# Performance work log

Hardware: AMD Instinct MI355X
Metric: run time of the kernel (lower is better)

Reference implementation:

```python
import jax, jax.numpy as jnp
import numpy as np

CODEBOOK_SIZE = 8192
EMBED_DIM = 256


def setup_inputs() -> dict:
    key = jax.random.key(0)
    k_rep, k_cb = jax.random.split(key)
    rep = jax.random.normal(k_rep, (32, 2048, EMBED_DIM), dtype=jnp.float32)
    codebook = jax.random.normal(k_cb, (CODEBOOK_SIZE, EMBED_DIM), dtype=jnp.float32)
    return {"rep": rep, "codebook": codebook}


def reference(rep, codebook):
    # rep: [B, M, D], codebook: [K, D]
    B, M, D = rep.shape
    rep_flat = rep.reshape(-1, D)                                # [B*M, D]
    a2 = jnp.sum(rep_flat * rep_flat, axis=1, keepdims=True)     # [B*M, 1]
    b2 = jnp.sum(codebook * codebook, axis=1)[None, :]           # [1, K]
    ab = rep_flat @ codebook.T                                   # [B*M, K]
    dist = a2 + b2 - 2.0 * ab                                    # [B*M, K]
    idx = jnp.argmin(dist, axis=1).reshape(B, M)                 # [B, M] int
    return idx
```

## Files before the change

kernel.cpp:

```cpp
#include <hip/hip_runtime.h>
#include <stdint.h>

#define KCODES 8192
#define DIM 256
#define BN 128
#define NKT (KCODES / BN)
#define NSTEP (NKT * 4)

typedef _Float16 h16;
typedef __attribute__((ext_vector_type(8))) _Float16 f16x8;
typedef __attribute__((ext_vector_type(4))) float f32x4;

__device__ __forceinline__ void split8(const float* __restrict__ x, f16x8& h, f16x8& l) {
    #pragma unroll
    for (int i = 0; i < 8; ++i) {
        float v = x[i];
        _Float16 hv = (_Float16)v;
        h[i] = hv;
        l[i] = (_Float16)(v - (float)hv);
    }
}

__device__ __forceinline__ unsigned int ford(float f) {
    unsigned int b = __float_as_uint(f);
    return (b & 0x80000000u) ? ~b : (b | 0x80000000u);
}

#define WS_C2H   0u
#define WS_LC    32768u
#define WS_CN    65536u
#define WS_CNT   98304u
#define WS_LIST  98560u
#define WS_CAND  360704u
#define WS_THR   622848u
#define WS_KEYS  917504u
#define WS_BPH   2097152u

__global__ __launch_bounds__(256) void c2x_kernel(const float* __restrict__ cb,
                                                  float* __restrict__ c2h,
                                                  float* __restrict__ lc,
                                                  float* __restrict__ cn, int K) {
    int w = (blockIdx.x * blockDim.x + threadIdx.x) >> 6;
    int lane = threadIdx.x & 63;
    if (w >= K) return;
    const float4 v = *(const float4*)(cb + (size_t)w * DIM + lane * 4);
    float s = 0.f, sr = 0.f;
    const float xs[4] = {v.x, v.y, v.z, v.w};
    #pragma unroll
    for (int i = 0; i < 4; ++i) {
        float x = xs[i];
        s += x * x;
        float hf = (float)(_Float16)x;
        float rho = x - hf;
        sr += rho * rho;
    }
    #pragma unroll
    for (int off = 32; off > 0; off >>= 1) { s += __shfl_down(s, off); sr += __shfl_down(sr, off); }
    if (lane == 0) { c2h[w] = 0.5f * s; cn[w] = sqrtf(s); lc[w] = sqrtf(sr); }
}

__global__ __launch_bounds__(256) void pack_h_kernel(const float* __restrict__ cb,
                                                     h16* __restrict__ Bp) {
    const int tid = blockIdx.x * 256 + threadIdx.x;
    const int code = tid >> 5;
    const int grp = tid & 31;
    float x[8];
    *(float4*)&x[0] = *(const float4*)(cb + (size_t)code * DIM + grp * 8);
    *(float4*)&x[4] = *(const float4*)(cb + (size_t)code * DIM + grp * 8 + 4);
    f16x8 hh;
    #pragma unroll
    for (int i = 0; i < 8; ++i) hh[i] = (_Float16)x[i];
    const int kt = code >> 7, col = code & 127;
    const int chunk = grp >> 2, g = grp & 3;
    const int P = kt * 4 + (chunk >> 1);
    const int s = (chunk & 1) * 4 + g;
    const int phys = s ^ (col & 7);
    *(f16x8*)(Bp + (size_t)P * 8192 + col * 64 + phys * 8) = hh;
}

__global__ __launch_bounds__(256, 3) void vq_pass1(
    const float* __restrict__ rep, const h16* __restrict__ Bp,
    const float* __restrict__ c2h, const float* __restrict__ lcA,
    const float* __restrict__ cnA, int* __restrict__ cand,
    float* __restrict__ thr) {

    __shared__ __align__(16) h16 ring[3][8192];

    const int t = threadIdx.x;
    const int lane = t & 63;
    const int c15 = lane & 15;
    const int g = lane >> 4;
    const int w = t >> 6;
    const int wrow = (w >> 1) * 32;
    const int wcol = (w & 1) * 64;
    const int row0 = blockIdx.x * 64;

    f16x8 ah[2][8];
    float hn[2], rn[2];
    #pragma unroll
    for (int m = 0; m < 2; ++m) {
        const float* ar = rep + (size_t)(row0 + wrow + m * 16 + c15) * DIM + g * 8;
        float hs = 0.f, rs = 0.f;
        #pragma unroll
        for (int ch = 0; ch < 8; ++ch) {
            float x[8];
            *(float4*)&x[0] = *(const float4*)(ar + ch * 32);
            *(float4*)&x[4] = *(const float4*)(ar + ch * 32 + 4);
            #pragma unroll
            for (int i = 0; i < 8; ++i) {
                _Float16 hv = (_Float16)x[i];
                ah[m][ch][i] = hv;
                float hf = (float)hv;
                hs += hf * hf;
                float rho = x[i] - hf;
                rs += rho * rho;
            }
        }
        hs += __shfl_xor(hs, 16); hs += __shfl_xor(hs, 32);
        rs += __shfl_xor(rs, 16); rs += __shfl_xor(rs, 32);
        hn[m] = sqrtf(hs); rn[m] = sqrtf(rs);
    }

    f32x4 acc[2][4];
    float u1v[2][4], u2v[2][4], B2[2][4];
    int u1i[2][4];
    #pragma unroll
    for (int m = 0; m < 2; ++m)
        #pragma unroll
        for (int n = 0; n < 4; ++n) {
            #pragma unroll
            for (int r = 0; r < 4; ++r) acc[m][n][r] = 0.f;
            u1v[m][n] = -3.4e38f; u2v[m][n] = -3.4e38f; u1i[m][n] = 0;
        }

    auto issueStep = [&](int s2, int slot) {
        const h16* src = Bp + (size_t)s2 * 8192 + t * 8;
        h16* dst = &ring[slot][t * 8];
        #pragma unroll
        for (int i = 0; i < 4; ++i)
            __builtin_amdgcn_global_load_lds(
                (const __attribute__((address_space(1))) uint32_t*)(src + i * 2048),
                (__attribute__((address_space(3))) uint32_t*)(dst + i * 2048),
                16, 0, 0);
    };

    asm volatile("s_waitcnt vmcnt(0)" ::: "memory");
    issueStep(0, 0);
    issueStep(1, 1);

    int bufq = 0;
    #pragma unroll 1
    for (int kt = 0; kt < NKT; ++kt) {
        const int ktbase = kt * BN;
        #pragma unroll
        for (int cp = 0; cp < 4; ++cp) {
            const int s = kt * 4 + cp;
            if (s == NSTEP - 1) asm volatile("s_waitcnt vmcnt(0) lgkmcnt(0)" ::: "memory");
            else                asm volatile("s_waitcnt vmcnt(4) lgkmcnt(0)" ::: "memory");
            __builtin_amdgcn_s_barrier();
            __builtin_amdgcn_sched_barrier(0);

            if (cp == 0) {
                #pragma unroll
                for (int n = 0; n < 4; ++n) {
                    const int col = ktbase + wcol + n * 16 + c15;
                    float cc = c2h[col], lv = lcA[col], cv = cnA[col];
                    #pragma unroll
                    for (int m = 0; m < 2; ++m)
                        B2[m][n] = hn[m] * lv + rn[m] * cv + 0.012f - cc;
                }
            }
            if (s + 2 < NSTEP) {
                int slot = bufq + 2;
                if (slot >= 3) slot -= 3;
                issueStep(s + 2, slot);
            }

            const h16* lb = &ring[bufq][0];
            #pragma unroll
            for (int j = 0; j < 2; ++j) {
                const int ch = cp * 2 + j;
                #pragma unroll
                for (int n = 0; n < 4; ++n) {
                    const int base = (wcol + n * 16 + c15) * 64;
                    f16x8 bh = *(const f16x8*)&lb[base + (((j * 4 + g) ^ (c15 & 7)) << 3)];
                    #pragma unroll
                    for (int m = 0; m < 2; ++m)
                        acc[m][n] = __builtin_amdgcn_mfma_f32_16x16x32_f16(ah[m][ch], bh, acc[m][n], 0, 0, 0);
                }
            }

            if (cp == 3) {
                #pragma unroll
                for (int n = 0; n < 4; ++n) {
                    const int col = ktbase + wcol + n * 16 + c15;
                    #pragma unroll
                    for (int m = 0; m < 2; ++m)
                        #pragma unroll
                        for (int r = 0; r < 4; ++r) {
                            float u = acc[m][n][r] + B2[m][n];
                            if (u > u1v[m][r]) { u2v[m][r] = u1v[m][r]; u1v[m][r] = u; u1i[m][r] = col; }
                            else if (u > u2v[m][r]) u2v[m][r] = u;
                            acc[m][n][r] = 0.f;
                        }
                }
            }
            bufq = (bufq + 1 == 3) ? 0 : bufq + 1;
        }
    }

    __syncthreads();
    float* sv1 = (float*)&ring[0][0];
    int* si1 = (int*)((char*)&ring[0][0] + 1024);
    float* sv2 = (float*)((char*)&ring[0][0] + 2048);
    #pragma unroll
    for (int m = 0; m < 2; ++m)
        #pragma unroll
        for (int r = 0; r < 4; ++r) {
            float a1 = u1v[m][r], a2 = u2v[m][r];
            int a1i = u1i[m][r];
            #pragma unroll
            for (int mask = 1; mask <= 8; mask <<= 1) {
                float b1 = __shfl_xor(a1, mask);
                int b1i = __shfl_xor(a1i, mask);
                float b2 = __shfl_xor(a2, mask);
                if (b1 > a1) { a2 = fmaxf(a1, b2); a1 = b1; a1i = b1i; }
                else         { a2 = fmaxf(b1, a2); }
            }
            if (c15 == 0) {
                const int rl = wrow + m * 16 + g * 4 + r;
                sv1[rl * 2 + (w & 1)] = a1;
                si1[rl * 2 + (w & 1)] = a1i;
                sv2[rl * 2 + (w & 1)] = a2;
            }
        }
    __syncthreads();
    if (t < 64) {
        float a1 = sv1[t * 2], a2 = sv2[t * 2];
        int a1i = si1[t * 2];
        float b1 = sv1[t * 2 + 1], b2 = sv2[t * 2 + 1];
        int b1i = si1[t * 2 + 1];
        float u1, u2; int u1idx;
        if (b1 > a1) { u1 = b1; u1idx = b1i; u2 = fmaxf(a1, b2); }
        else         { u1 = a1; u1idx = a1i; u2 = fmaxf(b1, a2); }
        cand[row0 + t] = u1idx;
        thr[row0 + t] = u2;
    }
}

__global__ __launch_bounds__(256) void resolve_kernel(
    const float* __restrict__ rep, const float* __restrict__ cb,
    const float* __restrict__ c2h, const int* __restrict__ cand,
    const float* __restrict__ thr, int* __restrict__ out,
    int* __restrict__ cnt, int* __restrict__ list, int N) {
    const int W = (blockIdx.x * 256 + threadIdx.x) >> 6;
    const int lane = threadIdx.x & 63;
    if (W >= N) return;
    const int ci = cand[W];
    const float4 rv = *(const float4*)(rep + (size_t)W * DIM + lane * 4);
    const float4 cv = *(const float4*)(cb + (size_t)ci * DIM + lane * 4);
    float p = rv.x * cv.x + rv.y * cv.y + rv.z * cv.z + rv.w * cv.w;
    #pragma unroll
    for (int off = 32; off > 0; off >>= 1) p += __shfl_down(p, off);
    if (lane == 0) {
        float sex = p - c2h[ci];
        out[W] = ci;
        if (!(sex > thr[W])) {
            int pos = atomicAdd(cnt, 1);
            list[pos] = W;
        }
    }
}

__global__ __launch_bounds__(256) void rescan_kernel(
    const float* __restrict__ rep, const float* __restrict__ cb,
    const float* __restrict__ c2h, const int* __restrict__ cnt_p,
    const int* __restrict__ list, unsigned long long* __restrict__ keys) {

    const int cnt = *cnt_p;
    const int base = blockIdx.x * 64;
    if (base >= cnt) return;
    const int nrows = min(64, cnt - base);
    const int ktbase = (int)blockIdx.y * BN;

    __shared__ __align__(16) h16 lds[2][BN * 64];
    const int t = threadIdx.x;
    const int lane = t & 63;
    const int w = t >> 6;
    const int c15 = lane & 15;
    const int g = lane >> 4;
    const int wrow = w * 16;

    const int aslot = wrow + c15;
    const int grow = list[base + (aslot < nrows ? aslot : 0)];
    f16x8 ah[8], al[8];
    {
        const float* ar = rep + (size_t)grow * DIM + g * 8;
        #pragma unroll
        for (int ch = 0; ch < 8; ++ch) {
            float x[8];
            *(float4*)&x[0] = *(const float4*)(ar + ch * 32);
            *(float4*)&x[4] = *(const float4*)(ar + ch * 32 + 4);
            split8(x, ah[ch], al[ch]);
        }
    }
    f32x4 acc[8];
    float cc[8];
    #pragma unroll
    for (int n = 0; n < 8; ++n) {
        #pragma unroll
        for (int r = 0; r < 4; ++r) acc[n][r] = 0.f;
        cc[n] = c2h[ktbase + n * 16 + c15];
    }

    const int scol = t >> 1;
    const int dslot = t & 1;
    float breg[16];
    auto loadB = [&](int ch) {
        const float* src = cb + (size_t)(ktbase + scol) * DIM + ch * 32 + dslot * 16;
        #pragma unroll
        for (int i = 0; i < 4; ++i) *(float4*)&breg[i * 4] = *(const float4*)(src + i * 4);
    };
    auto writeB = [&](int buf) {
        #pragma unroll
        for (int half = 0; half < 2; ++half) {
            f16x8 hh, ll;
            split8(&breg[half * 8], hh, ll);
            const int s = dslot * 2 + half;
            *(f16x8*)&lds[buf][scol * 64 + ((s ^ (scol & 7)) << 3)] = hh;
            *(f16x8*)&lds[buf][scol * 64 + (((s + 4) ^ (scol & 7)) << 3)] = ll;
        }
    };

    loadB(0);
    writeB(0);
    loadB(1);
    __syncthreads();

    #pragma unroll
    for (int chunk = 0; chunk < 8; ++chunk) {
        const int buf = chunk & 1;
        if (chunk != 7) writeB(buf ^ 1);
        if (chunk <= 5) loadB(chunk + 2);
        #pragma unroll
        for (int n = 0; n < 8; ++n) {
            const int bb = (n * 16 + c15) * 64;
            f16x8 bh = *(const f16x8*)&lds[buf][bb + ((g ^ (lane & 7)) << 3)];
            f16x8 bl = *(const f16x8*)&lds[buf][bb + (((4 + g) ^ (lane & 7)) << 3)];
            acc[n] = __builtin_amdgcn_mfma_f32_16x16x32_f16(ah[chunk], bh, acc[n], 0, 0, 0);
            acc[n] = __builtin_amdgcn_mfma_f32_16x16x32_f16(ah[chunk], bl, acc[n], 0, 0, 0);
            acc[n] = __builtin_amdgcn_mfma_f32_16x16x32_f16(al[chunk], bh, acc[n], 0, 0, 0);
            acc[n] = __builtin_amdgcn_mfma_f32_16x16x32_f16(al[chunk], bl, acc[n], 0, 0, 0);
        }
        __syncthreads();
    }

    #pragma unroll
    for (int r = 0; r < 4; ++r) {
        float bv = -3.4e38f;
        int bi = 0;
        #pragma unroll
        for (int n = 0; n < 8; ++n) {
            float s2 = acc[n][r] - cc[n];
            const int col = ktbase + n * 16 + c15;
            if (s2 > bv) { bv = s2; bi = col; }
        }
        #pragma unroll
        for (int mask = 1; mask <= 8; mask <<= 1) {
            float ov = __shfl_xor(bv, mask);
            int oi = __shfl_xor(bi, mask);
            if (ov > bv || (ov == bv && oi < bi)) { bv = ov; bi = oi; }
        }
        const int oslot = wrow + g * 4 + r;
        if (c15 == 0 && oslot < nrows) {
            unsigned long long key =
                ((unsigned long long)ford(bv) << 32) | (unsigned int)(~(unsigned int)bi);
            atomicMax(&keys[list[base + oslot]], key);
        }
    }
}

__global__ __launch_bounds__(256) void writeback_kernel(
    const int* __restrict__ cnt_p, const int* __restrict__ list,
    const unsigned long long* __restrict__ keys, int* __restrict__ out) {
    int i = blockIdx.x * 256 + threadIdx.x;
    if (i >= *cnt_p) return;
    int row = list[i];
    out[row] = (int)(~(unsigned int)(keys[row] & 0xFFFFFFFFull));
}

extern "C" void kernel_launch(void* const* d_in, const int* in_sizes, int n_in,
                              void* d_out, int out_size, void* d_ws, size_t ws_size,
                              hipStream_t stream) {
    const float* rep = (const float*)d_in[0];
    const float* cb = (const float*)d_in[1];
    const int N = in_sizes[0] / DIM;
    const int K = in_sizes[1] / DIM;
    char* ws = (char*)d_ws;
    float* c2h = (float*)(ws + WS_C2H);
    float* lc  = (float*)(ws + WS_LC);
    float* cn  = (float*)(ws + WS_CN);
    int* cnt   = (int*)(ws + WS_CNT);
    int* list  = (int*)(ws + WS_LIST);
    int* cand  = (int*)(ws + WS_CAND);
    float* thr = (float*)(ws + WS_THR);
    unsigned long long* keys = (unsigned long long*)(ws + WS_KEYS);
    h16* Bph   = (h16*)(ws + WS_BPH);
    int* out = (int*)d_out;

    c2x_kernel<<<dim3((K * 64 + 255) / 256), dim3(256), 0, stream>>>(cb, c2h, lc, cn, K);
    pack_h_kernel<<<dim3(KCODES * 32 / 256), dim3(256), 0, stream>>>(cb, Bph);
    hipMemsetAsync(cnt, 0, sizeof(int), stream);
    hipMemsetAsync(keys, 0, (size_t)N * sizeof(unsigned long long), stream);
    vq_pass1<<<dim3(N / 64), dim3(256), 0, stream>>>(rep, Bph, c2h, lc, cn, cand, thr);
    resolve_kernel<<<dim3(N / 4), dim3(256), 0, stream>>>(rep, cb, c2h, cand, thr, out, cnt, list, N);
    rescan_kernel<<<dim3(N / 64, NKT), dim3(256), 0, stream>>>(rep, cb, c2h, cnt, list, keys);
    writeback_kernel<<<dim3(N / 256), dim3(256), 0, stream>>>(cnt, list, keys, out);
}
```

Baseline: 524.8 us.

## Double rows per block and use global-max error bound in pass1

Each block in the first pass now handles 128 rows instead of 64, with each wave computing a 64x64 tile. Every LDS-loaded codebook fragment is therefore reused across four A fragments, which halves codebook traffic per row. The per-code error bound, built from per-code residual and norm values, is replaced by a row-only bound that uses the global maxima of those values, gathered with atomics in c2x. That bound is folded into the accumulator initial value, which removes per-tile bias loads and a separate add. The looser bound likely admits more ambiguous rows into the rescan path, and occupancy drops from 3 to 2 blocks because of higher register use.

```diff
diff --git a/kernel.cpp b/kernel.cpp
--- a/kernel.cpp
+++ b/kernel.cpp
@@ -39,7 +39,9 @@
 __global__ __launch_bounds__(256) void c2x_kernel(const float* __restrict__ cb,
                                                   float* __restrict__ c2h,
                                                   float* __restrict__ lc,
-                                                  float* __restrict__ cn, int K) {
+                                                  float* __restrict__ cn,
+                                                  unsigned int* __restrict__ gmx,
+                                                  int K) {
     int w = (blockIdx.x * blockDim.x + threadIdx.x) >> 6;
     int lane = threadIdx.x & 63;
     if (w >= K) return;
@@ -56,7 +58,12 @@
     }
     #pragma unroll
     for (int off = 32; off > 0; off >>= 1) { s += __shfl_down(s, off); sr += __shfl_down(sr, off); }
-    if (lane == 0) { c2h[w] = 0.5f * s; cn[w] = sqrtf(s); lc[w] = sqrtf(sr); }
+    if (lane == 0) {
+        float sn = sqrtf(s), srn = sqrtf(sr);
+        c2h[w] = 0.5f * s; cn[w] = sn; lc[w] = srn;
+        atomicMax(&gmx[0], __float_as_uint(srn));
+        atomicMax(&gmx[1], __float_as_uint(sn));
+    }
 }
 
 __global__ __launch_bounds__(256) void pack_h_kernel(const float* __restrict__ cb,
@@ -78,11 +85,10 @@
     *(f16x8*)(Bp + (size_t)P * 8192 + col * 64 + phys * 8) = hh;
 }
 
-__global__ __launch_bounds__(256, 3) void vq_pass1(
+__global__ __launch_bounds__(256, 2) void vq_pass1(
     const float* __restrict__ rep, const h16* __restrict__ Bp,
-    const float* __restrict__ c2h, const float* __restrict__ lcA,
-    const float* __restrict__ cnA, int* __restrict__ cand,
-    float* __restrict__ thr) {
+    const float* __restrict__ c2h, const unsigned int* __restrict__ gmx,
+    int* __restrict__ cand, float* __restrict__ thr) {
 
     __shared__ __align__(16) h16 ring[3][8192];
 
@@ -91,14 +97,17 @@
     const int c15 = lane & 15;
     const int g = lane >> 4;
     const int w = t >> 6;
-    const int wrow = (w >> 1) * 32;
+    const int wrow = (w >> 1) * 64;
     const int wcol = (w & 1) * 64;
-    const int row0 = blockIdx.x * 64;
-
-    f16x8 ah[2][8];
-    float hn[2], rn[2];
-    #pragma unroll
-    for (int m = 0; m < 2; ++m) {
+    const int row0 = blockIdx.x * 128;
+
+    const float Lmax = __uint_as_float(gmx[0]);
+    const float Cmax = __uint_as_float(gmx[1]);
+
+    f16x8 ah[4][8];
+    float U[4][4];
+    #pragma unroll
+    for (int m = 0; m < 4; ++m) {
         const float* ar = rep + (size_t)(row0 + wrow + m * 16 + c15) * DIM + g * 8;
         float hs = 0.f, rs = 0.f;
         #pragma unroll
@@ -118,20 +127,22 @@
         }
         hs += __shfl_xor(hs, 16); hs += __shfl_xor(hs, 32);
         rs += __shfl_xor(rs, 16); rs += __shfl_xor(rs, 32);
-        hn[m] = sqrtf(hs); rn[m] = sqrtf(rs);
-    }
-
-    f32x4 acc[2][4];
-    float u1v[2][4], u2v[2][4], B2[2][4];
-    int u1i[2][4];
-    #pragma unroll
-    for (int m = 0; m < 2; ++m)
-        #pragma unroll
-        for (int n = 0; n < 4; ++n) {
-            #pragma unroll
-            for (int r = 0; r < 4; ++r) acc[m][n][r] = 0.f;
-            u1v[m][n] = -3.4e38f; u2v[m][n] = -3.4e38f; u1i[m][n] = 0;
-        }
+        float hn = sqrtf(hs), rn = sqrtf(rs);
+        #pragma unroll
+        for (int r = 0; r < 4; ++r) {
+            float hnr = __shfl(hn, g * 4 + r);
+            float rnr = __shfl(rn, g * 4 + r);
+            U[m][r] = fmaf(hnr, Lmax, fmaf(rnr, Cmax, 0.012f));
+        }
+    }
+
+    f32x4 acc[4][4];
+    float u1v[4][4], u2v[4][4], D[4];
+    int u1i[4][4];
+    #pragma unroll
+    for (int m = 0; m < 4; ++m)
+        #pragma unroll
+        for (int r = 0; r < 4; ++r) { u1v[m][r] = -3.4e38f; u2v[m][r] = -3.4e38f; u1i[m][r] = 0; }
 
     auto issueStep = [&](int s2, int slot) {
         const h16* src = Bp + (size_t)s2 * 8192 + t * 8;
@@ -162,13 +173,13 @@
 
             if (cp == 0) {
                 #pragma unroll
-                for (int n = 0; n < 4; ++n) {
-                    const int col = ktbase + wcol + n * 16 + c15;
-                    float cc = c2h[col], lv = lcA[col], cv = cnA[col];
+                for (int n = 0; n < 4; ++n) D[n] = c2h[ktbase + wcol + n * 16 + c15];
+                #pragma unroll
+                for (int m = 0; m < 4; ++m)
                     #pragma unroll
-                    for (int m = 0; m < 2; ++m)
-                        B2[m][n] = hn[m] * lv + rn[m] * cv + 0.012f - cc;
-                }
+                    for (int n = 0; n < 4; ++n)
+                        #pragma unroll
+                        for (int r = 0; r < 4; ++r) acc[m][n][r] = U[m][r];
             }
             if (s + 2 < NSTEP) {
                 int slot = bufq + 2;
@@ -179,14 +190,15 @@
             const h16* lb = &ring[bufq][0];
             #pragma unroll
             for (int j = 0; j < 2; ++j) {
-                const int ch = cp * 2 + j;
                 #pragma unroll
                 for (int n = 0; n < 4; ++n) {
                     const int base = (wcol + n * 16 + c15) * 64;
                     f16x8 bh = *(const f16x8*)&lb[base + (((j * 4 + g) ^ (c15 & 7)) << 3)];
                     #pragma unroll
-                    for (int m = 0; m < 2; ++m)
+                    for (int m = 0; m < 4; ++m) {
+                        const int ch = cp * 2 + j;
                         acc[m][n] = __builtin_amdgcn_mfma_f32_16x16x32_f16(ah[m][ch], bh, acc[m][n], 0, 0, 0);
+                    }
                 }
             }
 
@@ -195,13 +207,12 @@
                 for (int n = 0; n < 4; ++n) {
                     const int col = ktbase + wcol + n * 16 + c15;
                     #pragma unroll
-                    for (int m = 0; m < 2; ++m)
+                    for (int m = 0; m < 4; ++m)
                         #pragma unroll
                         for (int r = 0; r < 4; ++r) {
-                            float u = acc[m][n][r] + B2[m][n];
+                            float u = acc[m][n][r] - D[n];
                             if (u > u1v[m][r]) { u2v[m][r] = u1v[m][r]; u1v[m][r] = u; u1i[m][r] = col; }
                             else if (u > u2v[m][r]) u2v[m][r] = u;
-                            acc[m][n][r] = 0.f;
                         }
                 }
             }
@@ -214,7 +225,7 @@
     int* si1 = (int*)((char*)&ring[0][0] + 1024);
     float* sv2 = (float*)((char*)&ring[0][0] + 2048);
     #pragma unroll
-    for (int m = 0; m < 2; ++m)
+    for (int m = 0; m < 4; ++m)
         #pragma unroll
         for (int r = 0; r < 4; ++r) {
             float a1 = u1v[m][r], a2 = u2v[m][r];
@@ -235,7 +246,7 @@
             }
         }
     __syncthreads();
-    if (t < 64) {
+    if (t < 128) {
         float a1 = sv1[t * 2], a2 = sv2[t * 2];
         int a1i = si1[t * 2];
         float b1 = sv1[t * 2 + 1], b2 = sv2[t * 2 + 1];
@@ -401,6 +412,7 @@
     float* lc  = (float*)(ws + WS_LC);
     float* cn  = (float*)(ws + WS_CN);
     int* cnt   = (int*)(ws + WS_CNT);
+    unsigned int* gmx = (unsigned int*)(ws + WS_CNT + 4);
     int* list  = (int*)(ws + WS_LIST);
     int* cand  = (int*)(ws + WS_CAND);
     float* thr = (float*)(ws + WS_THR);
@@ -408,11 +420,11 @@
     h16* Bph   = (h16*)(ws + WS_BPH);
     int* out = (int*)d_out;
 
-    c2x_kernel<<<dim3((K * 64 + 255) / 256), dim3(256), 0, stream>>>(cb, c2h, lc, cn, K);
+    hipMemsetAsync(ws + WS_CNT, 0, 64, stream);
+    hipMemsetAsync(keys, 0, (size_t)N * sizeof(unsigned long long), stream);
+    c2x_kernel<<<dim3((K * 64 + 255) / 256), dim3(256), 0, stream>>>(cb, c2h, lc, cn, gmx, K);
     pack_h_kernel<<<dim3(KCODES * 32 / 256), dim3(256), 0, stream>>>(cb, Bph);
-    hipMemsetAsync(cnt, 0, sizeof(int), stream);
-    hipMemsetAsync(keys, 0, (size_t)N * sizeof(unsigned long long), stream);
-    vq_pass1<<<dim3(N / 64), dim3(256), 0, stream>>>(rep, Bph, c2h, lc, cn, cand, thr);
+    vq_pass1<<<dim3(N / 128), dim3(256), 0, stream>>>(rep, Bph, c2h, gmx, cand, thr);
     resolve_kernel<<<dim3(N / 4), dim3(256), 0, stream>>>(rep, cb, c2h, cand, thr, out, cnt, list, N);
     rescan_kernel<<<dim3(N / 64, NKT), dim3(256), 0, stream>>>(rep, cb, c2h, cnt, list, keys);
     writeback_kernel<<<dim3(N / 256), dim3(256), 0, stream>>>(cnt, list, keys, out);
```

Result: slower. 852.6 us (+62.5%).

## Fuse codebook prep kernels and use global-max error bound in pass1

Applied to the files above, without the earlier changes.

Merges the norm and fp16-pack kernels into one prep kernel that also atomically records the maximum codebook norm and fp16 residual norm. Pass1 then uses a per-row error bound built from those global maxima, seeded directly into the accumulators, in place of per-code bound terms loaded each tile. This cuts per-tile loads and registers. Pass1 also drops from a three-slot to a two-slot LDS ring and raises the occupancy hint from 3 to 5, at the cost of a full vmcnt(0) wait each step. The looser bound may send more rows to the rescan path.

```diff
diff --git a/kernel.cpp b/kernel.cpp
--- a/kernel.cpp
+++ b/kernel.cpp
@@ -27,8 +27,6 @@
 }
 
 #define WS_C2H   0u
-#define WS_LC    32768u
-#define WS_CN    65536u
 #define WS_CNT   98304u
 #define WS_LIST  98560u
 #define WS_CAND  360704u
@@ -36,31 +34,10 @@
 #define WS_KEYS  917504u
 #define WS_BPH   2097152u
 
-__global__ __launch_bounds__(256) void c2x_kernel(const float* __restrict__ cb,
-                                                  float* __restrict__ c2h,
-                                                  float* __restrict__ lc,
-                                                  float* __restrict__ cn, int K) {
-    int w = (blockIdx.x * blockDim.x + threadIdx.x) >> 6;
-    int lane = threadIdx.x & 63;
-    if (w >= K) return;
-    const float4 v = *(const float4*)(cb + (size_t)w * DIM + lane * 4);
-    float s = 0.f, sr = 0.f;
-    const float xs[4] = {v.x, v.y, v.z, v.w};
-    #pragma unroll
-    for (int i = 0; i < 4; ++i) {
-        float x = xs[i];
-        s += x * x;
-        float hf = (float)(_Float16)x;
-        float rho = x - hf;
-        sr += rho * rho;
-    }
-    #pragma unroll
-    for (int off = 32; off > 0; off >>= 1) { s += __shfl_down(s, off); sr += __shfl_down(sr, off); }
-    if (lane == 0) { c2h[w] = 0.5f * s; cn[w] = sqrtf(s); lc[w] = sqrtf(sr); }
-}
-
-__global__ __launch_bounds__(256) void pack_h_kernel(const float* __restrict__ cb,
-                                                     h16* __restrict__ Bp) {
+__global__ __launch_bounds__(256) void prep_kernel(const float* __restrict__ cb,
+                                                   h16* __restrict__ Bp,
+                                                   float* __restrict__ c2h,
+                                                   unsigned int* __restrict__ gmx) {
     const int tid = blockIdx.x * 256 + threadIdx.x;
     const int code = tid >> 5;
     const int grp = tid & 31;
@@ -68,23 +45,41 @@
     *(float4*)&x[0] = *(const float4*)(cb + (size_t)code * DIM + grp * 8);
     *(float4*)&x[4] = *(const float4*)(cb + (size_t)code * DIM + grp * 8 + 4);
     f16x8 hh;
-    #pragma unroll
-    for (int i = 0; i < 8; ++i) hh[i] = (_Float16)x[i];
+    float s = 0.f, sr = 0.f;
+    #pragma unroll
+    for (int i = 0; i < 8; ++i) {
+        float v = x[i];
+        _Float16 hv = (_Float16)v;
+        hh[i] = hv;
+        s += v * v;
+        float rho = v - (float)hv;
+        sr += rho * rho;
+    }
     const int kt = code >> 7, col = code & 127;
     const int chunk = grp >> 2, g = grp & 3;
     const int P = kt * 4 + (chunk >> 1);
-    const int s = (chunk & 1) * 4 + g;
-    const int phys = s ^ (col & 7);
+    const int sl = (chunk & 1) * 4 + g;
+    const int phys = sl ^ (col & 7);
     *(f16x8*)(Bp + (size_t)P * 8192 + col * 64 + phys * 8) = hh;
-}
-
-__global__ __launch_bounds__(256, 3) void vq_pass1(
+
+    #pragma unroll
+    for (int off = 16; off > 0; off >>= 1) {
+        s += __shfl_xor(s, off);
+        sr += __shfl_xor(sr, off);
+    }
+    if (grp == 0) {
+        c2h[code] = 0.5f * s;
+        atomicMax(&gmx[0], __float_as_uint(sqrtf(sr)));
+        atomicMax(&gmx[1], __float_as_uint(sqrtf(s)));
+    }
+}
+
+__global__ __launch_bounds__(256, 5) void vq_pass1(
     const float* __restrict__ rep, const h16* __restrict__ Bp,
-    const float* __restrict__ c2h, const float* __restrict__ lcA,
-    const float* __restrict__ cnA, int* __restrict__ cand,
-    float* __restrict__ thr) {
-
-    __shared__ __align__(16) h16 ring[3][8192];
+    const float* __restrict__ c2h, const unsigned int* __restrict__ gmx,
+    int* __restrict__ cand, float* __restrict__ thr) {
+
+    __shared__ __align__(16) h16 buf[2][8192];
 
     const int t = threadIdx.x;
     const int lane = t & 63;
@@ -95,8 +90,11 @@
     const int wcol = (w & 1) * 64;
     const int row0 = blockIdx.x * 64;
 
+    const float Lmax = __uint_as_float(gmx[0]);
+    const float Cmax = __uint_as_float(gmx[1]);
+
     f16x8 ah[2][8];
-    float hn[2], rn[2];
+    float U[2][4];
     #pragma unroll
     for (int m = 0; m < 2; ++m) {
         const float* ar = rep + (size_t)(row0 + wrow + m * 16 + c15) * DIM + g * 8;
@@ -118,24 +116,26 @@
         }
         hs += __shfl_xor(hs, 16); hs += __shfl_xor(hs, 32);
         rs += __shfl_xor(rs, 16); rs += __shfl_xor(rs, 32);
-        hn[m] = sqrtf(hs); rn[m] = sqrtf(rs);
+        float hn = sqrtf(hs), rn = sqrtf(rs);
+        #pragma unroll
+        for (int r = 0; r < 4; ++r) {
+            float hnr = __shfl(hn, g * 4 + r);
+            float rnr = __shfl(rn, g * 4 + r);
+            U[m][r] = fmaf(hnr, Lmax, fmaf(rnr, Cmax, 0.012f));
+        }
     }
 
     f32x4 acc[2][4];
-    float u1v[2][4], u2v[2][4], B2[2][4];
+    float u1v[2][4], u2v[2][4], D[4];
     int u1i[2][4];
     #pragma unroll
     for (int m = 0; m < 2; ++m)
         #pragma unroll
-        for (int n = 0; n < 4; ++n) {
-            #pragma unroll
-            for (int r = 0; r < 4; ++r) acc[m][n][r] = 0.f;
-            u1v[m][n] = -3.4e38f; u2v[m][n] = -3.4e38f; u1i[m][n] = 0;
-        }
-
-    auto issueStep = [&](int s2, int slot) {
+        for (int r = 0; r < 4; ++r) { u1v[m][r] = -3.4e38f; u2v[m][r] = -3.4e38f; u1i[m][r] = 0; }
+
+    auto issueStep = [&](int s2, int b) {
         const h16* src = Bp + (size_t)s2 * 8192 + t * 8;
-        h16* dst = &ring[slot][t * 8];
+        h16* dst = &buf[b][t * 8];
         #pragma unroll
         for (int i = 0; i < 4; ++i)
             __builtin_amdgcn_global_load_lds(
@@ -144,39 +144,32 @@
                 16, 0, 0);
     };
 
-    asm volatile("s_waitcnt vmcnt(0)" ::: "memory");
     issueStep(0, 0);
-    issueStep(1, 1);
-
-    int bufq = 0;
+
     #pragma unroll 1
     for (int kt = 0; kt < NKT; ++kt) {
         const int ktbase = kt * BN;
         #pragma unroll
         for (int cp = 0; cp < 4; ++cp) {
             const int s = kt * 4 + cp;
-            if (s == NSTEP - 1) asm volatile("s_waitcnt vmcnt(0) lgkmcnt(0)" ::: "memory");
-            else                asm volatile("s_waitcnt vmcnt(4) lgkmcnt(0)" ::: "memory");
+            const int par = cp & 1;
+            asm volatile("s_waitcnt vmcnt(0) lgkmcnt(0)" ::: "memory");
             __builtin_amdgcn_s_barrier();
             __builtin_amdgcn_sched_barrier(0);
 
             if (cp == 0) {
                 #pragma unroll
-                for (int n = 0; n < 4; ++n) {
-                    const int col = ktbase + wcol + n * 16 + c15;
-                    float cc = c2h[col], lv = lcA[col], cv = cnA[col];
+                for (int n = 0; n < 4; ++n) D[n] = c2h[ktbase + wcol + n * 16 + c15];
+                #pragma unroll
+                for (int m = 0; m < 2; ++m)
                     #pragma unroll
-                    for (int m = 0; m < 2; ++m)
-                        B2[m][n] = hn[m] * lv + rn[m] * cv + 0.012f - cc;
-                }
-            }
-            if (s + 2 < NSTEP) {
-                int slot = bufq + 2;
-                if (slot >= 3) slot -= 3;
-                issueStep(s + 2, slot);
-            }
-
-            const h16* lb = &ring[bufq][0];
+                    for (int n = 0; n < 4; ++n)
+                        #pragma unroll
+                        for (int r = 0; r < 4; ++r) acc[m][n][r] = U[m][r];
+            }
+            if (s + 1 < NSTEP) issueStep(s + 1, par ^ 1);
+
+            const h16* lb = &buf[par][0];
             #pragma unroll
             for (int j = 0; j < 2; ++j) {
                 const int ch = cp * 2 + j;
@@ -198,21 +191,19 @@
                     for (int m = 0; m < 2; ++m)
                         #pragma unroll
                         for (int r = 0; r < 4; ++r) {
-                            float u = acc[m][n][r] + B2[m][n];
+                            float u = acc[m][n][r] - D[n];
                             if (u > u1v[m][r]) { u2v[m][r] = u1v[m][r]; u1v[m][r] = u; u1i[m][r] = col; }
                             else if (u > u2v[m][r]) u2v[m][r] = u;
-                            acc[m][n][r] = 0.f;
                         }
                 }
             }
-            bufq = (bufq + 1 == 3) ? 0 : bufq + 1;
         }
     }
 
     __syncthreads();
-    float* sv1 = (float*)&ring[0][0];
-    int* si1 = (int*)((char*)&ring[0][0] + 1024);
-    float* sv2 = (float*)((char*)&ring[0][0] + 2048);
+    float* sv1 = (float*)&buf[0][0];
+    int* si1 = (int*)((char*)&buf[0][0] + 1024);
+    float* sv2 = (float*)((char*)&buf[0][0] + 2048);
     #pragma unroll
     for (int m = 0; m < 2; ++m)
         #pragma unroll
@@ -396,11 +387,11 @@
     const float* cb = (const float*)d_in[1];
     const int N = in_sizes[0] / DIM;
     const int K = in_sizes[1] / DIM;
+    (void)K;
     char* ws = (char*)d_ws;
     float* c2h = (float*)(ws + WS_C2H);
-    float* lc  = (float*)(ws + WS_LC);
-    float* cn  = (float*)(ws + WS_CN);
     int* cnt   = (int*)(ws + WS_CNT);
+    unsigned int* gmx = (unsigned int*)(ws + WS_CNT + 4);
     int* list  = (int*)(ws + WS_LIST);
     int* cand  = (int*)(ws + WS_CAND);
     float* thr = (float*)(ws + WS_THR);
@@ -408,11 +399,10 @@
     h16* Bph   = (h16*)(ws + WS_BPH);
     int* out = (int*)d_out;
 
-    c2x_kernel<<<dim3((K * 64 + 255) / 256), dim3(256), 0, stream>>>(cb, c2h, lc, cn, K);
-    pack_h_kernel<<<dim3(KCODES * 32 / 256), dim3(256), 0, stream>>>(cb, Bph);
-    hipMemsetAsync(cnt, 0, sizeof(int), stream);
+    hipMemsetAsync(ws + WS_CNT, 0, 64, stream);
     hipMemsetAsync(keys, 0, (size_t)N * sizeof(unsigned long long), stream);
-    vq_pass1<<<dim3(N / 64), dim3(256), 0, stream>>>(rep, Bph, c2h, lc, cn, cand, thr);
+    prep_kernel<<<dim3(KCODES * 32 / 256), dim3(256), 0, stream>>>(cb, Bph, c2h, gmx);
+    vq_pass1<<<dim3(N / 64), dim3(256), 0, stream>>>(rep, Bph, c2h, gmx, cand, thr);
     resolve_kernel<<<dim3(N / 4), dim3(256), 0, stream>>>(rep, cb, c2h, cand, thr, out, cnt, list, N);
     rescan_kernel<<<dim3(N / 64, NKT), dim3(256), 0, stream>>>(rep, cb, c2h, cnt, list, keys);
     writeback_kernel<<<dim3(N / 256), dim3(256), 0, stream>>>(cnt, list, keys, out);
```

After: 989.7 us. +88.6%, slower.
